# Kernel optimization log

Measured on AMD Instinct MI355X. Metric: run time of the kernel, lower is better.

## Reference

```python
import jax, jax.numpy as jnp
import numpy as np

NUM_HEADS = 16
HIDDEN = 1024
HEAD = HIDDEN // NUM_HEADS
SCALE = float(np.sqrt(HEAD))


def relu6(x):
    return jnp.minimum(jax.nn.relu(x), 6.0)


def setup_inputs() -> dict:
    key = jax.random.key(0)
    ks = jax.random.split(key, 9)
    T_t, T_s, B = 2048, 2048, 4
    init = 1.0 / np.sqrt(HIDDEN)  # torch Linear default uniform(-1/sqrt(fan_in), ...)
    return {
        "q": jax.random.normal(ks[0], (T_t, B, HIDDEN), jnp.float32),
        "k": jax.random.normal(ks[1], (T_s, B, HIDDEN), jnp.float32),
        "v": jax.random.normal(ks[2], (T_s, B, HIDDEN), jnp.float32),
        "Wq": jax.random.uniform(ks[3], (HIDDEN, HIDDEN), jnp.float32, -init, init),
        "bq": jax.random.uniform(ks[4], (HIDDEN,), jnp.float32, -init, init),
        "Wk": jax.random.uniform(ks[5], (HIDDEN, HIDDEN), jnp.float32, -init, init),
        "bk": jax.random.uniform(ks[6], (HIDDEN,), jnp.float32, -init, init),
        "Wv": jax.random.uniform(ks[7], (HIDDEN, HIDDEN), jnp.float32, -init, init),
        "bv": jax.random.uniform(ks[8], (HIDDEN,), jnp.float32, -init, init),
    }


def reference(q, k, v, Wq, bq, Wk, bk, Wv, bv):
    T_t, B, _ = q.shape
    T_s = k.shape[0]
    # QKV projections with ReLU6 (torch Linear: x @ W.T + b), then split heads
    qh = relu6(q @ Wq.T + bq).reshape(T_t, B, NUM_HEADS, HEAD)  # (T_t,B,h,d)
    kh = relu6(k @ Wk.T + bk).reshape(T_s, B, NUM_HEADS, HEAD)  # (T_s,B,h,d)
    vh = relu6(v @ Wv.T + bv).reshape(T_s, B, NUM_HEADS, HEAD)  # (T_s,B,h,d)
    # scores: (B,h,T_t,T_s)
    scores = jnp.einsum("tbhd,sbhd->bhts", qh, kh) / SCALE
    attn = jax.nn.softmax(scores, axis=-1)  # dropout is identity in eval mode
    out = jnp.einsum("bhts,sbhd->tbhd", attn, vh)  # (T_t,B,h,d)
    return out.reshape(T_t, B, NUM_HEADS * HEAD)
```

## Files before the change

### kernel.cpp

```cpp
#include <hip/hip_runtime.h>
#include <hip/hip_bf16.h>
#include <math.h>

#define HIDDEN 1024
#define NH 16
#define HD 64
#define TT 2048
#define NB 4
#define MROWS (TT*NB)
#define HEADSZ (TT*HD)

typedef __attribute__((ext_vector_type(8))) __bf16 bf16x8;
typedef __attribute__((ext_vector_type(2))) __bf16 bf16x2;
typedef __attribute__((ext_vector_type(8))) unsigned short u16x8;
typedef __attribute__((ext_vector_type(4))) float f32x4;
typedef __attribute__((ext_vector_type(4))) unsigned int u32x4;

__device__ __forceinline__ unsigned short f2bf(float x) {
  union { float f; unsigned int u; } v; v.f = x;
  unsigned int r = v.u + 0x7fffu + ((v.u >> 16) & 1u);
  return (unsigned short)(r >> 16);
}

__device__ __forceinline__ unsigned int packpair(float a, float b) {
#if __has_builtin(__builtin_amdgcn_cvt_pk_bf16_f32)
  bf16x2 t = __builtin_amdgcn_cvt_pk_bf16_f32(a, b);
  return __builtin_bit_cast(unsigned int, t);
#else
  return (unsigned int)f2bf(a) | ((unsigned int)f2bf(b) << 16);
#endif
}

__device__ __forceinline__ bf16x8 ld_frag(const unsigned short* p) {
  return __builtin_bit_cast(bf16x8, *(const u16x8*)p);
}

__device__ __forceinline__ void gload16(const void* g, void* l) {
  __builtin_amdgcn_global_load_lds(
      (const __attribute__((address_space(1))) void*)g,
      (__attribute__((address_space(3))) void*)l, 16, 0, 0);
}

__device__ __forceinline__ void stage32(const unsigned short* gp, unsigned short* lp) {
#pragma unroll
  for (int u = 0; u < 4; u++)
    *(u16x8*)(lp + u * 8) = *(const u16x8*)(gp + u * 8);
}
__device__ __forceinline__ void stage32(const float* gp, unsigned short* lp) {
#pragma unroll
  for (int u = 0; u < 4; u++) {
    float4 a0 = *(const float4*)(gp + u * 8);
    float4 a1 = *(const float4*)(gp + u * 8 + 4);
    u32x4 pk;
    pk.x = packpair(a0.x, a0.y); pk.y = packpair(a0.z, a0.w);
    pk.z = packpair(a1.x, a1.y); pk.w = packpair(a1.z, a1.w);
    *(u32x4*)(lp + u * 8) = pk;
  }
}

__global__ __launch_bounds__(256)
void cvt_kernel(const float* __restrict__ s, unsigned short* __restrict__ d, int n4) {
  int i = blockIdx.x * 256 + threadIdx.x;
  if (i >= n4) return;
  float4 f = ((const float4*)s)[i];
  unsigned int lo = packpair(f.x, f.y), hi = packpair(f.z, f.w);
  ((uint2*)d)[i] = make_uint2(lo, hi);
}

__global__ __launch_bounds__(256)
void cvt3_kernel(const float* __restrict__ a, const float* __restrict__ b,
                 const float* __restrict__ c, unsigned short* __restrict__ d,
                 int n4, long long stride4) {
  const float* s = (blockIdx.y == 0) ? a : (blockIdx.y == 1) ? b : c;
  int i = blockIdx.x * 256 + threadIdx.x;
  if (i >= n4) return;
  float4 f = ((const float4*)s)[i];
  unsigned int lo = packpair(f.x, f.y), hi = packpair(f.z, f.w);
  ((uint2*)d)[(size_t)blockIdx.y * stride4 + i] = make_uint2(lo, hi);
}

__global__ __launch_bounds__(256)
void projg3_kernel(const unsigned short* __restrict__ Xb,
                   const unsigned short* __restrict__ Wb,
                   const float* __restrict__ bq, const float* __restrict__ bk,
                   const float* __restrict__ bv,
                   unsigned short* __restrict__ outq, unsigned short* __restrict__ outk,
                   unsigned short* __restrict__ outv)
{
  __shared__ __align__(16) unsigned short As[128 * 64];
  __shared__ __align__(16) unsigned short Bs[128 * 64];

  const int z = blockIdx.z;
  const unsigned short* Xp = Xb + (size_t)z * ((size_t)MROWS * HIDDEN);
  const unsigned short* Wp = Wb + (size_t)z * ((size_t)HIDDEN * HIDDEN);
  const float* bias = (z == 0) ? bq : (z == 1) ? bk : bv;
  unsigned short* out = (z == 0) ? outq : (z == 1) ? outk : outv;

  const int tid = threadIdx.x;
  const int lane = tid & 63;
  const int w = tid >> 6;
  const int wm = w & 1, wn = w >> 1;
  const int lr = lane & 15, lq = lane >> 4;
  const int bm = blockIdx.y, bn = blockIdx.x;

  const int srow = lane >> 3;
  const int schunk = (lane & 7) * 8;

  const unsigned short* Ag = Xp + (size_t)(bm * 128 + w * 32 + srow) * HIDDEN + schunk;
  const unsigned short* Bg = Wp + (size_t)(bn * 128 + w * 32 + srow) * HIDDEN + schunk;
  unsigned short* Al = &As[w * 32 * 64];
  unsigned short* Bl = &Bs[w * 32 * 64];

  f32x4 acc[4][4];
#pragma unroll
  for (int i = 0; i < 4; i++)
#pragma unroll
    for (int j = 0; j < 4; j++) acc[i][j] = (f32x4){0.f, 0.f, 0.f, 0.f};

  for (int k0 = 0; k0 < HIDDEN; k0 += 64) {
#pragma unroll
    for (int u = 0; u < 4; u++) {
      gload16(Ag + k0 + u * 8 * HIDDEN, Al + u * 512);
      gload16(Bg + k0 + u * 8 * HIDDEN, Bl + u * 512);
    }
    __syncthreads();
#pragma unroll
    for (int kk = 0; kk < 64; kk += 32) {
      bf16x8 af[4], bfr[4];
#pragma unroll
      for (int i = 0; i < 4; i++)
        af[i] = ld_frag(&As[(wm * 64 + i * 16 + lr) * 64 + kk + lq * 8]);
#pragma unroll
      for (int j = 0; j < 4; j++)
        bfr[j] = ld_frag(&Bs[(wn * 64 + j * 16 + lr) * 64 + kk + lq * 8]);
#pragma unroll
      for (int i = 0; i < 4; i++)
#pragma unroll
        for (int j = 0; j < 4; j++)
          acc[i][j] = __builtin_amdgcn_mfma_f32_16x16x32_bf16(af[i], bfr[j], acc[i][j], 0, 0, 0);
    }
    __syncthreads();
  }

#pragma unroll
  for (int j = 0; j < 4; j++) {
    const int n = bn * 128 + wn * 64 + j * 16 + lr;
    const float bb = bias[n];
    const int h = n >> 6, d = n & 63;
#pragma unroll
    for (int i = 0; i < 4; i++) {
      const int mb = bm * 128 + wm * 64 + i * 16 + lq * 4;
#pragma unroll
      for (int r = 0; r < 4; r++) {
        const int m = mb + r;
        const int t = m >> 2, b = m & 3;
        float vv = acc[i][j][r] + bb;
        vv = fminf(fmaxf(vv, 0.0f), 6.0f);
        if (z == 2) {
          const int s = t;
          const int st = s >> 7, sl = s & 127;
          const int a = (sl & 15) * 8 + (sl >> 4);
          out[(size_t)(b * NH + h) * HEADSZ + (size_t)d * TT + st * 128 + a] = f2bf(vv);
        } else {
          out[(size_t)(b * NH + h) * HEADSZ + (size_t)t * HD + d] = f2bf(vv);
        }
      }
    }
  }
}

template<int VT>
__global__ __launch_bounds__(256)
void projg_kernel(const unsigned short* __restrict__ Xp, const unsigned short* __restrict__ Wp,
                  const float* __restrict__ bias, unsigned short* __restrict__ out)
{
  __shared__ __align__(16) unsigned short As[128 * 64];
  __shared__ __align__(16) unsigned short Bs[128 * 64];

  const int tid = threadIdx.x;
  const int lane = tid & 63;
  const int w = tid >> 6;
  const int wm = w & 1, wn = w >> 1;
  const int lr = lane & 15, lq = lane >> 4;
  const int bm = blockIdx.y, bn = blockIdx.x;

  const int srow = lane >> 3;
  const int schunk = (lane & 7) * 8;

  const unsigned short* Ag = Xp + (size_t)(bm * 128 + w * 32 + srow) * HIDDEN + schunk;
  const unsigned short* Bg = Wp + (size_t)(bn * 128 + w * 32 + srow) * HIDDEN + schunk;
  unsigned short* Al = &As[w * 32 * 64];
  unsigned short* Bl = &Bs[w * 32 * 64];

  f32x4 acc[4][4];
#pragma unroll
  for (int i = 0; i < 4; i++)
#pragma unroll
    for (int j = 0; j < 4; j++) acc[i][j] = (f32x4){0.f, 0.f, 0.f, 0.f};

  for (int k0 = 0; k0 < HIDDEN; k0 += 64) {
#pragma unroll
    for (int u = 0; u < 4; u++) {
      gload16(Ag + k0 + u * 8 * HIDDEN, Al + u * 512);
      gload16(Bg + k0 + u * 8 * HIDDEN, Bl + u * 512);
    }
    __syncthreads();
#pragma unroll
    for (int kk = 0; kk < 64; kk += 32) {
      bf16x8 af[4], bfr[4];
#pragma unroll
      for (int i = 0; i < 4; i++)
        af[i] = ld_frag(&As[(wm * 64 + i * 16 + lr) * 64 + kk + lq * 8]);
#pragma unroll
      for (int j = 0; j < 4; j++)
        bfr[j] = ld_frag(&Bs[(wn * 64 + j * 16 + lr) * 64 + kk + lq * 8]);
#pragma unroll
      for (int i = 0; i < 4; i++)
#pragma unroll
        for (int j = 0; j < 4; j++)
          acc[i][j] = __builtin_amdgcn_mfma_f32_16x16x32_bf16(af[i], bfr[j], acc[i][j], 0, 0, 0);
    }
    __syncthreads();
  }

#pragma unroll
  for (int j = 0; j < 4; j++) {
    const int n = bn * 128 + wn * 64 + j * 16 + lr;
    const float bb = bias[n];
    const int h = n >> 6, d = n & 63;
#pragma unroll
    for (int i = 0; i < 4; i++) {
      const int mb = bm * 128 + wm * 64 + i * 16 + lq * 4;
#pragma unroll
      for (int r = 0; r < 4; r++) {
        const int m = mb + r;
        const int t = m >> 2, b = m & 3;
        float vv = acc[i][j][r] + bb;
        vv = fminf(fmaxf(vv, 0.0f), 6.0f);
        if (VT) {
          const int s = t;
          const int st = s >> 7, sl = s & 127;
          const int a = (sl & 15) * 8 + (sl >> 4);
          out[(size_t)(b * NH + h) * HEADSZ + (size_t)d * TT + st * 128 + a] = f2bf(vv);
        } else {
          out[(size_t)(b * NH + h) * HEADSZ + (size_t)t * HD + d] = f2bf(vv);
        }
      }
    }
  }
}

#define PLD 72

template<int VT, typename XT, typename WT>
__global__ __launch_bounds__(256, 3)
void proj_kernel(const XT* __restrict__ Xp, const WT* __restrict__ Wp,
                 const float* __restrict__ bias, unsigned short* __restrict__ out)
{
  __shared__ unsigned short As[128 * PLD];
  __shared__ unsigned short Bs[128 * PLD];

  const int tid = threadIdx.x;
  const int lane = tid & 63;
  const int wid = tid >> 6;
  const int wm = wid & 1, wn = wid >> 1;
  const int lr = lane & 15, lq = lane >> 4;
  const int bm = blockIdx.y, bn = blockIdx.x;

  const int srow = tid >> 1;
  const int scol = (tid & 1) * 32;

  const XT* Ap = Xp + (size_t)(bm * 128 + srow) * HIDDEN + scol;
  const WT* Bp = Wp + (size_t)(bn * 128 + srow) * HIDDEN + scol;
  unsigned short* Asw = &As[srow * PLD + scol];
  unsigned short* Bsw = &Bs[srow * PLD + scol];

  f32x4 acc[4][4];
#pragma unroll
  for (int i = 0; i < 4; i++)
#pragma unroll
    for (int j = 0; j < 4; j++) acc[i][j] = (f32x4){0.f, 0.f, 0.f, 0.f};

  for (int k0 = 0; k0 < HIDDEN; k0 += 64) {
    stage32(Ap + k0, Asw);
    stage32(Bp + k0, Bsw);
    __syncthreads();
#pragma unroll
    for (int kk = 0; kk < 64; kk += 32) {
      bf16x8 af[4], bfr[4];
#pragma unroll
      for (int i = 0; i < 4; i++)
        af[i] = ld_frag(&As[(wm * 64 + i * 16 + lr) * PLD + kk + lq * 8]);
#pragma unroll
      for (int j = 0; j < 4; j++)
        bfr[j] = ld_frag(&Bs[(wn * 64 + j * 16 + lr) * PLD + kk + lq * 8]);
#pragma unroll
      for (int i = 0; i < 4; i++)
#pragma unroll
        for (int j = 0; j < 4; j++)
          acc[i][j] = __builtin_amdgcn_mfma_f32_16x16x32_bf16(af[i], bfr[j], acc[i][j], 0, 0, 0);
    }
    __syncthreads();
  }

#pragma unroll
  for (int j = 0; j < 4; j++) {
    const int n = bn * 128 + wn * 64 + j * 16 + lr;
    const float bb = bias[n];
    const int h = n >> 6, d = n & 63;
#pragma unroll
    for (int i = 0; i < 4; i++) {
      const int mb = bm * 128 + wm * 64 + i * 16 + lq * 4;
#pragma unroll
      for (int r = 0; r < 4; r++) {
        const int m = mb + r;
        const int t = m >> 2, b = m & 3;
        float vv = acc[i][j][r] + bb;
        vv = fminf(fmaxf(vv, 0.0f), 6.0f);
        if (VT) {
          const int s = t;
          const int st = s >> 7, sl = s & 127;
          const int a = (sl & 15) * 8 + (sl >> 4);
          out[(size_t)(b * NH + h) * HEADSZ + (size_t)d * TT + st * 128 + a] = f2bf(vv);
        } else {
          out[(size_t)(b * NH + h) * HEADSZ + (size_t)t * HD + d] = f2bf(vv);
        }
      }
    }
  }
}

#define QLD 72
#define PLDS 136
#define VLD 136
#define MBIAS 24.0f

__global__ __launch_bounds__(256, 3)
void attn_kernel(const unsigned short* __restrict__ qh,
                 const unsigned short* __restrict__ kh,
                 const unsigned short* __restrict__ vh,
                 float* __restrict__ outp)
{
  __shared__ unsigned short KPs[128 * PLDS];
  __shared__ unsigned short Vt[64 * VLD];

  const int tid = threadIdx.x;
  const int lane = tid & 63;
  const int w = tid >> 6;
  const int lr = lane & 15, lq = lane >> 4;
  const int qt = blockIdx.x, bh = blockIdx.y;
  const int b = bh >> 4, h = bh & 15;
  const int t0 = qt * 128;

  const size_t headoff = (size_t)bh * HEADSZ;

  {
    const unsigned short* qb = qh + headoff + (size_t)t0 * HD;
    const int row = tid >> 1, c0 = (tid & 1) * 32;
    stage32(qb + (size_t)row * HD + c0, &KPs[row * QLD + c0]);
  }
  __syncthreads();
  bf16x8 aq[2][2];
#pragma unroll
  for (int i = 0; i < 2; i++)
#pragma unroll
    for (int kx = 0; kx < 2; kx++)
      aq[i][kx] = ld_frag(&KPs[(w * 32 + i * 16 + lr) * QLD + kx * 32 + lq * 8]);
  __syncthreads();

  union { u16x8 v; unsigned short s[8]; } uo;
  const unsigned short ov = (lr == 0) ? (unsigned short)0x3F80 : (unsigned short)0;
#pragma unroll
  for (int z = 0; z < 8; z++) uo.s[z] = ov;
  const bf16x8 onesf = __builtin_bit_cast(bf16x8, uo.v);

  f32x4 Oacc[2][4];
  f32x4 lacc[2];
#pragma unroll
  for (int i = 0; i < 2; i++) {
#pragma unroll
    for (int jo = 0; jo < 4; jo++) Oacc[i][jo] = (f32x4){0.f, 0.f, 0.f, 0.f};
    lacc[i] = (f32x4){0.f, 0.f, 0.f, 0.f};
  }

  const float csc = 0.1803368801111204f;

  for (int st = 0; st < TT / 128; st++) {
    {
      const unsigned short* kb = kh + headoff + (size_t)st * (128 * HD);
      const int row = tid >> 1, c0 = (tid & 1) * 32;
      stage32(kb + (size_t)row * HD + c0, &KPs[row * QLD + c0]);
    }
    {
      const unsigned short* vb = vh + headoff + st * 128;
      const int dd = tid >> 2, a0 = (tid & 3) * 32;
#pragma unroll
      for (int u = 0; u < 4; u++)
        *(u16x8*)&Vt[dd * VLD + a0 + u * 8] = *(const u16x8*)(vb + (size_t)dd * TT + a0 + u * 8);
    }
    __syncthreads();

    f32x4 sc[2][8];
#pragma unroll
    for (int i = 0; i < 2; i++)
#pragma unroll
      for (int j = 0; j < 8; j++) sc[i][j] = (f32x4){0.f, 0.f, 0.f, 0.f};

    __builtin_amdgcn_s_setprio(1);
#pragma unroll
    for (int kx = 0; kx < 2; kx++) {
#pragma unroll
      for (int j = 0; j < 8; j++) {
        bf16x8 bk = ld_frag(&KPs[(j * 16 + lr) * QLD + kx * 32 + lq * 8]);
#pragma unroll
        for (int i = 0; i < 2; i++)
          sc[i][j] = __builtin_amdgcn_mfma_f32_16x16x32_bf16(aq[i][kx], bk, sc[i][j], 0, 0, 0);
      }
    }
    __builtin_amdgcn_s_setprio(0);
    __syncthreads();

#pragma unroll
    for (int i = 0; i < 2; i++)
#pragma unroll
      for (int j = 0; j < 8; j++)
#pragma unroll
        for (int r = 0; r < 4; r++)
          sc[i][j][r] = exp2f(fmaf(sc[i][j][r], csc, -MBIAS));

#pragma unroll
    for (int i = 0; i < 2; i++)
#pragma unroll
      for (int r = 0; r < 4; r++) {
        const int row = w * 32 + i * 16 + lq * 4 + r;
        u32x4 pk;
        pk.x = packpair(sc[i][0][r], sc[i][1][r]);
        pk.y = packpair(sc[i][2][r], sc[i][3][r]);
        pk.z = packpair(sc[i][4][r], sc[i][5][r]);
        pk.w = packpair(sc[i][6][r], sc[i][7][r]);
        *(u16x8*)&KPs[row * PLDS + lr * 8] = __builtin_bit_cast(u16x8, pk);
      }
    __syncthreads();

    __builtin_amdgcn_s_setprio(1);
#pragma unroll
    for (int ks = 0; ks < 128; ks += 32) {
      bf16x8 ap[2];
#pragma unroll
      for (int i = 0; i < 2; i++)
        ap[i] = ld_frag(&KPs[(w * 32 + i * 16 + lr) * PLDS + ks + lq * 8]);
#pragma unroll
      for (int jo = 0; jo < 4; jo++) {
        bf16x8 bv2 = ld_frag(&Vt[(jo * 16 + lr) * VLD + ks + lq * 8]);
#pragma unroll
        for (int i = 0; i < 2; i++)
          Oacc[i][jo] = __builtin_amdgcn_mfma_f32_16x16x32_bf16(ap[i], bv2, Oacc[i][jo], 0, 0, 0);
      }
#pragma unroll
      for (int i = 0; i < 2; i++)
        lacc[i] = __builtin_amdgcn_mfma_f32_16x16x32_bf16(ap[i], onesf, lacc[i], 0, 0, 0);
    }
    __builtin_amdgcn_s_setprio(0);
    __syncthreads();
  }

#pragma unroll
  for (int i = 0; i < 2; i++)
#pragma unroll
    for (int r = 0; r < 4; r++) {
      const float l = __shfl(lacc[i][r], lane & 48);
      const float inv = 1.0f / l;
      const int t = t0 + w * 32 + i * 16 + lq * 4 + r;
      float* op = outp + ((size_t)t * NB + b) * HIDDEN + h * HD;
#pragma unroll
      for (int jo = 0; jo < 4; jo++)
        op[jo * 16 + lr] = Oacc[i][jo][r] * inv;
    }
}

extern "C" void kernel_launch(void* const* d_in, const int* in_sizes, int n_in,
                              void* d_out, int out_size, void* d_ws, size_t ws_size,
                              hipStream_t stream)
{
  const float* q  = (const float*)d_in[0];
  const float* k  = (const float*)d_in[1];
  const float* v  = (const float*)d_in[2];
  const float* Wq = (const float*)d_in[3];
  const float* bq = (const float*)d_in[4];
  const float* Wk = (const float*)d_in[5];
  const float* bk = (const float*)d_in[6];
  const float* Wv = (const float*)d_in[7];
  const float* bv = (const float*)d_in[8];

  const size_t actN = (size_t)MROWS * HIDDEN;
  const size_t WN   = (size_t)HIDDEN * HIDDEN;
  unsigned short* qh  = (unsigned short*)d_ws;
  unsigned short* kh  = qh + actN;
  unsigned short* vh  = kh + actN;
  unsigned short* Wb3 = vh + actN;
  unsigned short* Xb3 = Wb3 + 3 * WN;

  const size_t need_fused = (6 * actN + 3 * WN) * 2;
  const size_t need_full  = (4 * actN + WN) * 2;
  const size_t need_w     = (3 * actN + WN) * 2;

  const int n4a = (int)(actN / 4);
  const int n4w = (int)(WN / 4);
  dim3 cga((n4a + 255) / 256), cgw((n4w + 255) / 256);
  dim3 pg(HIDDEN / 128, MROWS / 128);
  dim3 pf(HIDDEN / 128, MROWS / 128, 3);
  dim3 ag(TT / 128, NB * NH);

  if (ws_size >= need_fused) {
    dim3 cw(cgw.x, 3), cx(cga.x, 3);
    cvt3_kernel<<<cw, 256, 0, stream>>>(Wq, Wk, Wv, Wb3, n4w, (long long)(WN / 4));
    cvt3_kernel<<<cx, 256, 0, stream>>>(q, k, v, Xb3, n4a, (long long)(actN / 4));
    projg3_kernel<<<pf, 256, 0, stream>>>(Xb3, Wb3, bq, bk, bv, qh, kh, vh);
  } else if (ws_size >= need_full) {
    unsigned short* Wbf = vh + actN;
    unsigned short* Xbf = Wbf + WN;
    cvt_kernel<<<cga, 256, 0, stream>>>(q, Xbf, n4a);
    cvt_kernel<<<cgw, 256, 0, stream>>>(Wq, Wbf, n4w);
    projg_kernel<0><<<pg, 256, 0, stream>>>(Xbf, Wbf, bq, qh);
    cvt_kernel<<<cga, 256, 0, stream>>>(k, Xbf, n4a);
    cvt_kernel<<<cgw, 256, 0, stream>>>(Wk, Wbf, n4w);
    projg_kernel<0><<<pg, 256, 0, stream>>>(Xbf, Wbf, bk, kh);
    cvt_kernel<<<cga, 256, 0, stream>>>(v, Xbf, n4a);
    cvt_kernel<<<cgw, 256, 0, stream>>>(Wv, Wbf, n4w);
    projg_kernel<1><<<pg, 256, 0, stream>>>(Xbf, Wbf, bv, vh);
  } else if (ws_size >= need_w) {
    unsigned short* Wbf = vh + actN;
    cvt_kernel<<<cgw, 256, 0, stream>>>(Wq, Wbf, n4w);
    proj_kernel<0, float, unsigned short><<<pg, 256, 0, stream>>>(q, Wbf, bq, qh);
    cvt_kernel<<<cgw, 256, 0, stream>>>(Wk, Wbf, n4w);
    proj_kernel<0, float, unsigned short><<<pg, 256, 0, stream>>>(k, Wbf, bk, kh);
    cvt_kernel<<<cgw, 256, 0, stream>>>(Wv, Wbf, n4w);
    proj_kernel<1, float, unsigned short><<<pg, 256, 0, stream>>>(v, Wbf, bv, vh);
  } else {
    proj_kernel<0, float, float><<<pg, 256, 0, stream>>>(q, Wq, bq, qh);
    proj_kernel<0, float, float><<<pg, 256, 0, stream>>>(k, Wk, bk, kh);
    proj_kernel<1, float, float><<<pg, 256, 0, stream>>>(v, Wv, bv, vh);
  }

  attn_kernel<<<ag, 256, 0, stream>>>(qh, kh, vh, (float*)d_out);
}
```

Measured before the change: 387.7 us.

## Double-buffer LDS in fused QKV projection GEMM and swizzle block order

Turns the fused QKV projection GEMM into a two-stage LDS pipeline: while the MFMAs run on the current 64-wide K slice, the next slice is already being loaded into the other buffer, and the second barrier per iteration is dropped. The 3D grid becomes a 1D grid of 1536 blocks with an XCD-style swizzle, so that neighbouring blocks sharing a row tile land together and get better L2 reuse. This doubles LDS use to 64KB per block, which may lower occupancy. The loads are asynchronous gload16 calls, so correctness depends on the barrier placement.

```diff
diff --git a/kernel.cpp b/kernel.cpp
--- a/kernel.cpp
+++ b/kernel.cpp
@@ -79,18 +79,52 @@
   ((uint2*)d)[(size_t)blockIdx.y * stride4 + i] = make_uint2(lo, hi);
 }
 
+__device__ __forceinline__ void pstage(const unsigned short* Ag, const unsigned short* Bg,
+                                       unsigned short* Al, unsigned short* Bl, int k0) {
+#pragma unroll
+  for (int u = 0; u < 4; u++) {
+    gload16(Ag + k0 + u * 8 * HIDDEN, Al + u * 512);
+    gload16(Bg + k0 + u * 8 * HIDDEN, Bl + u * 512);
+  }
+}
+
+__device__ __forceinline__ void pcomp(const unsigned short* Ab, const unsigned short* Bb,
+                                      int wm, int wn, int lr, int lq, f32x4 (&acc)[4][4]) {
+#pragma unroll
+  for (int kk = 0; kk < 64; kk += 32) {
+    bf16x8 af[4], bfr[4];
+#pragma unroll
+    for (int i = 0; i < 4; i++)
+      af[i] = ld_frag(&Ab[(wm * 64 + i * 16 + lr) * 64 + kk + lq * 8]);
+#pragma unroll
+    for (int j = 0; j < 4; j++)
+      bfr[j] = ld_frag(&Bb[(wn * 64 + j * 16 + lr) * 64 + kk + lq * 8]);
+#pragma unroll
+    for (int i = 0; i < 4; i++)
+#pragma unroll
+      for (int j = 0; j < 4; j++)
+        acc[i][j] = __builtin_amdgcn_mfma_f32_16x16x32_bf16(af[i], bfr[j], acc[i][j], 0, 0, 0);
+  }
+}
+
 __global__ __launch_bounds__(256)
-void projg3_kernel(const unsigned short* __restrict__ Xb,
-                   const unsigned short* __restrict__ Wb,
-                   const float* __restrict__ bq, const float* __restrict__ bk,
-                   const float* __restrict__ bv,
-                   unsigned short* __restrict__ outq, unsigned short* __restrict__ outk,
-                   unsigned short* __restrict__ outv)
+void projp_kernel(const unsigned short* __restrict__ Xb,
+                  const unsigned short* __restrict__ Wb,
+                  const float* __restrict__ bq, const float* __restrict__ bk,
+                  const float* __restrict__ bv,
+                  unsigned short* __restrict__ outq, unsigned short* __restrict__ outk,
+                  unsigned short* __restrict__ outv)
 {
-  __shared__ __align__(16) unsigned short As[128 * 64];
-  __shared__ __align__(16) unsigned short Bs[128 * 64];
-
-  const int z = blockIdx.z;
+  __shared__ __align__(16) unsigned short As[2][128 * 64];
+  __shared__ __align__(16) unsigned short Bs[2][128 * 64];
+
+  const int id = blockIdx.x;
+  const int swz = (id & 7) * 192 + (id >> 3);
+  const int z = swz >> 9;
+  const int rem = swz & 511;
+  const int bm = rem >> 3;
+  const int bn = rem & 7;
+
   const unsigned short* Xp = Xb + (size_t)z * ((size_t)MROWS * HIDDEN);
   const unsigned short* Wp = Wb + (size_t)z * ((size_t)HIDDEN * HIDDEN);
   const float* bias = (z == 0) ? bq : (z == 1) ? bk : bv;
@@ -101,15 +135,13 @@
   const int w = tid >> 6;
   const int wm = w & 1, wn = w >> 1;
   const int lr = lane & 15, lq = lane >> 4;
-  const int bm = blockIdx.y, bn = blockIdx.x;
 
   const int srow = lane >> 3;
   const int schunk = (lane & 7) * 8;
 
   const unsigned short* Ag = Xp + (size_t)(bm * 128 + w * 32 + srow) * HIDDEN + schunk;
   const unsigned short* Bg = Wp + (size_t)(bn * 128 + w * 32 + srow) * HIDDEN + schunk;
-  unsigned short* Al = &As[w * 32 * 64];
-  unsigned short* Bl = &Bs[w * 32 * 64];
+  const int wl = w * 32 * 64;
 
   f32x4 acc[4][4];
 #pragma unroll
@@ -117,30 +149,16 @@
 #pragma unroll
     for (int j = 0; j < 4; j++) acc[i][j] = (f32x4){0.f, 0.f, 0.f, 0.f};
 
-  for (int k0 = 0; k0 < HIDDEN; k0 += 64) {
-#pragma unroll
-    for (int u = 0; u < 4; u++) {
-      gload16(Ag + k0 + u * 8 * HIDDEN, Al + u * 512);
-      gload16(Bg + k0 + u * 8 * HIDDEN, Bl + u * 512);
-    }
-    __syncthreads();
-#pragma unroll
-    for (int kk = 0; kk < 64; kk += 32) {
-      bf16x8 af[4], bfr[4];
-#pragma unroll
-      for (int i = 0; i < 4; i++)
-        af[i] = ld_frag(&As[(wm * 64 + i * 16 + lr) * 64 + kk + lq * 8]);
-#pragma unroll
-      for (int j = 0; j < 4; j++)
-        bfr[j] = ld_frag(&Bs[(wn * 64 + j * 16 + lr) * 64 + kk + lq * 8]);
-#pragma unroll
-      for (int i = 0; i < 4; i++)
-#pragma unroll
-        for (int j = 0; j < 4; j++)
-          acc[i][j] = __builtin_amdgcn_mfma_f32_16x16x32_bf16(af[i], bfr[j], acc[i][j], 0, 0, 0);
-    }
-    __syncthreads();
-  }
+  pstage(Ag, Bg, &As[0][wl], &Bs[0][wl], 0);
+  __syncthreads();
+  for (int ks = 0; ks < 15; ks++) {
+    const int cur = ks & 1, nxt = cur ^ 1;
+    pstage(Ag, Bg, &As[nxt][wl], &Bs[nxt][wl], (ks + 1) * 64);
+    __builtin_amdgcn_sched_barrier(0);
+    pcomp(As[cur], Bs[cur], wm, wn, lr, lq, acc);
+    __syncthreads();
+  }
+  pcomp(As[1], Bs[1], wm, wn, lr, lq, acc);
 
 #pragma unroll
   for (int j = 0; j < 4; j++) {
@@ -508,14 +526,13 @@
   const int n4w = (int)(WN / 4);
   dim3 cga((n4a + 255) / 256), cgw((n4w + 255) / 256);
   dim3 pg(HIDDEN / 128, MROWS / 128);
-  dim3 pf(HIDDEN / 128, MROWS / 128, 3);
   dim3 ag(TT / 128, NB * NH);
 
   if (ws_size >= need_fused) {
     dim3 cw(cgw.x, 3), cx(cga.x, 3);
     cvt3_kernel<<<cw, 256, 0, stream>>>(Wq, Wk, Wv, Wb3, n4w, (long long)(WN / 4));
     cvt3_kernel<<<cx, 256, 0, stream>>>(q, k, v, Xb3, n4a, (long long)(actN / 4));
-    projg3_kernel<<<pf, 256, 0, stream>>>(Xb3, Wb3, bq, bk, bv, qh, kh, vh);
+    projp_kernel<<<dim3(1536), 256, 0, stream>>>(Xb3, Wb3, bq, bk, bv, qh, kh, vh);
   } else if (ws_size >= need_full) {
     unsigned short* Wbf = vh + actN;
     unsigned short* Xbf = Wbf + WN;
```

Result: slower. 410.5 us (+5.9%).
